# Optimization experiments

Measured on AMD Instinct MI355X. Metric: run time of the kernel, lower is better.

## Reference

```python
import jax, jax.numpy as jnp
import numpy as np

IN_DIM = 768
OUT_DIM = 768


def setup_inputs() -> dict:
    key = jax.random.key(0)
    k_x, k_q, k_k, k_v = jax.random.split(key, 4)
    B, S = 4, 4096
    x = jax.random.normal(k_x, (B, S, IN_DIM), dtype=jnp.float32)
    scale = 1.0 / np.sqrt(IN_DIM)
    Wq = jax.random.normal(k_q, (IN_DIM, OUT_DIM), dtype=jnp.float32) * scale
    Wk = jax.random.normal(k_k, (IN_DIM, OUT_DIM), dtype=jnp.float32) * scale
    Wv = jax.random.normal(k_v, (IN_DIM, OUT_DIM), dtype=jnp.float32) * scale
    return {"x": x, "Wq": Wq, "Wk": Wk, "Wv": Wv}


def reference(x, Wq, Wk, Wv):
    # x: [B, S, D_in]; W*: [D_in, D_out] (Linear without bias)
    q = jnp.einsum('bsd,de->bse', x, Wq)
    k = jnp.einsum('bsd,de->bse', x, Wk)
    v = jnp.einsum('bsd,de->bse', x, Wv)
    S = x.shape[1]
    scores = jnp.einsum('bqe,bke->bqk', q, k)  # [B, S, S]
    causal = jnp.tril(jnp.ones((S, S), dtype=bool))  # True where allowed
    scores = jnp.where(causal[None], scores, -jnp.inf)
    scale = 1.0 / jnp.sqrt(jnp.asarray(q.shape[-1], dtype=scores.dtype))
    weights = jax.nn.softmax(scores * scale, axis=-1)
    # dropout p=0.0 -> identity
    return jnp.einsum('bqk,bke->bqe', weights, v)
```

## Files before the change

kernel.cpp:

```cpp
#include <hip/hip_runtime.h>
#include <hip/hip_bf16.h>
#include <hip/hip_fp16.h>

#define DIM 768
#define SLEN 4096
#define BATCH 4
#define NTILES 528
#define NT256 136

typedef __attribute__((ext_vector_type(8))) short short8;
typedef __attribute__((ext_vector_type(4))) short short4v;
typedef __attribute__((ext_vector_type(4))) float f32x4;
typedef __attribute__((ext_vector_type(8))) _Float16 f16x8;

typedef __attribute__((address_space(1))) void gvoid;
typedef __attribute__((address_space(3))) void lvoid;

__device__ __forceinline__ void gl_lds16(const void* g, void* l) {
  __builtin_amdgcn_global_load_lds((gvoid*)g, (lvoid*)l, 16, 0, 0);
}

__device__ __forceinline__ unsigned short f2h(float x) {
  union { _Float16 h; unsigned short u; } c; c.h = (_Float16)x; return c.u;
}
__device__ __forceinline__ float h2f(unsigned short u) {
  union { _Float16 h; unsigned short u; } c; c.u = u; return (float)c.h;
}

union V8 { short8 v; unsigned short u[8]; };

__global__ __launch_bounds__(256) void convert_x_kernel(
    const float* __restrict__ x, unsigned short* __restrict__ xb) {
  size_t i = ((size_t)blockIdx.x * 256 + threadIdx.x) * 8;
  f32x4 a = *(const f32x4*)(x + i);
  f32x4 b = *(const f32x4*)(x + i + 4);
  V8 o;
#pragma unroll
  for (int j = 0; j < 4; ++j) { o.u[j] = f2h(a[j]); o.u[4 + j] = f2h(b[j]); }
  *(short8*)(xb + i) = o.v;
}

__global__ __launch_bounds__(256) void transpose_w_kernel(
    const float* __restrict__ Wq, const float* __restrict__ Wk,
    const float* __restrict__ Wv, unsigned short* __restrict__ Wt) {
  __shared__ float Tl[32][33];
  const float* Wi = blockIdx.z == 0 ? Wq : (blockIdx.z == 1 ? Wk : Wv);
  unsigned short* Wo = Wt + (size_t)blockIdx.z * DIM * DIM;
  int k0 = blockIdx.x * 32, n0 = blockIdx.y * 32;
  int t = threadIdx.x;
  int r = t >> 3, c4 = (t & 7) * 4;
  f32x4 v = *(const f32x4*)(Wi + (size_t)(k0 + r) * DIM + n0 + c4);
#pragma unroll
  for (int j = 0; j < 4; ++j) Tl[r][c4 + j] = v[j];
  __syncthreads();
  short4v ov;
#pragma unroll
  for (int j = 0; j < 4; ++j) ov[j] = (short)f2h(Tl[c4 + j][r]);
  *(short4v*)(Wo + (size_t)(n0 + r) * DIM + k0 + c4) = ov;
}


#define STAGE(src, row0, kb, ldsoff)                                              \
  {                                                                               \
    gl_lds16((src) + (size_t)((row0) + rA) * DIM + (kb) + cA,                     \
             ldsb + (ldsoff) + t * 16);                                           \
    gl_lds16((src) + (size_t)((row0) + 64 + rA) * DIM + (kb) + cA,                \
             ldsb + (ldsoff) + 8192 + t * 16);                                    \
  }

#define QPHASE(MH, CHB, STG, VMW)                                                 \
  {                                                                               \
    f16x8 afr[4];                                                                 \
    _Pragma("unroll") for (int j = 0; j < 4; ++j)                                 \
        afr[j] = __builtin_bit_cast(f16x8, *(const short8*)(ldsb + aB +           \
                 (MH) * 16384 + (j * 32 + arow) * 128 + (CHB)));                  \
    if ((MH) == 0) {                                                              \
      _Pragma("unroll") for (int n = 0; n < 4; ++n)                               \
          bfr[n] = __builtin_bit_cast(f16x8, *(const short8*)(ldsb + bB +         \
                   bh * 16384 + (brow + n * 16) * 128 + (CHB)));                  \
    }                                                                             \
    STG;                                                                          \
    VMW;                                                                          \
    asm volatile("s_barrier" ::: "memory");                                       \
    asm volatile("s_waitcnt lgkmcnt(0)" ::: "memory");                            \
    __builtin_amdgcn_sched_barrier(0);                                            \
    __builtin_amdgcn_s_setprio(1);                                                \
    _Pragma("unroll") for (int j = 0; j < 4; ++j)                                 \
      _Pragma("unroll") for (int n = 0; n < 4; ++n)                               \
        acc[(MH) * 4 + j][n] = __builtin_amdgcn_mfma_f32_16x16x32_f16(            \
            afr[j], bfr[n], acc[(MH) * 4 + j][n], 0, 0, 0);                       \
    __builtin_amdgcn_s_setprio(0);                                                \
    __builtin_amdgcn_sched_barrier(0);                                            \
    asm volatile("s_barrier" ::: "memory");                                       \
  }

template <int MODE>
__global__ __launch_bounds__(512, 2) void gemm8_kernel(
    const unsigned short* __restrict__ Ag, const unsigned short* __restrict__ Bg,
    unsigned short* __restrict__ o0, unsigned short* __restrict__ o1,
    unsigned short* __restrict__ o2, size_t stAB, size_t stS) {
  __shared__ __align__(16) unsigned short lds[65536];
  char* ldsb = (char*)lds;
  const int t = threadIdx.x;
  const int lane = t & 63, w = t >> 6;
  const int l15 = lane & 15, lg = lane >> 4;
  const int wr = w >> 2, wc = w & 3;

  int m0, n0, qt = 0, kt = 0;
  const unsigned short *A, *B;
  unsigned short* Co = nullptr;
  unsigned short* Sb = nullptr;
  if (MODE == 0) {
    m0 = blockIdx.x * 256; n0 = blockIdx.y * 256;
    A = Ag; B = Bg + (size_t)blockIdx.z * DIM * DIM;
    Co = blockIdx.z == 0 ? o0 : (blockIdx.z == 1 ? o1 : o2);
  } else {
    const int i = blockIdx.x, b = blockIdx.y;
    qt = (int)((sqrtf(8.f * i + 1.f) - 1.f) * 0.5f);
    while ((qt + 1) * (qt + 2) / 2 <= i) ++qt;
    while (qt * (qt + 1) / 2 > i) --qt;
    kt = i - qt * (qt + 1) / 2;
    m0 = qt * 256; n0 = kt * 256;
    A = Ag + (size_t)b * stAB; B = Bg + (size_t)b * stAB;
    Sb = o0 + (size_t)b * stS;
  }

  const int rA = t >> 3;
  const int cA = (((t & 7) ^ ((t >> 3) & 7)) << 3);
  const int ch0 = ((lg ^ (l15 & 7)) << 4);
  const int arow = wr * 16 + l15;
  const int bh = wc >> 1;
  const int brow = (wc & 1) * 64 + l15;

  f32x4 acc[8][4];
#pragma unroll
  for (int f = 0; f < 8; ++f)
#pragma unroll
    for (int n = 0; n < 4; ++n) acc[f][n] = f32x4{0.f, 0.f, 0.f, 0.f};

  STAGE(A, m0, 0, 0);
  STAGE(B, n0, 0, 65536);
  STAGE(B, n0 + 128, 0, 65536 + 16384);
  STAGE(A, m0 + 128, 0, 16384);
  STAGE(A, m0, 64, 32768);
  asm volatile("s_waitcnt vmcnt(4)" ::: "memory");
  asm volatile("s_barrier" ::: "memory");

  for (int tt = 0; tt < 12; ++tt) {
    const int bt = tt & 1;
    const int aB = bt * 32768;
    const int bB = 65536 + bt * 32768;
    const int aN = (1 - bt) * 32768;
    const int bN = 65536 + (1 - bt) * 32768;
    const int kb1 = (tt + 1 < 12 ? tt + 1 : 11) * 64;
    const int kb2 = (tt + 2 < 12 ? tt + 2 : 11) * 64;
    f16x8 bfr[4];
    QPHASE(0, ch0, STAGE(B, n0, kb1, bN),
           asm volatile("s_waitcnt vmcnt(4)" ::: "memory"));
    QPHASE(1, ch0, STAGE(B, n0 + 128, kb1, bN + 16384), (void)0);
    QPHASE(0, ch0 ^ 64, STAGE(A, m0 + 128, kb1, aN + 16384), (void)0);
    QPHASE(1, ch0 ^ 64, STAGE(A, m0, kb2, aB),
           asm volatile("s_waitcnt vmcnt(4)" ::: "memory"));
  }
  asm volatile("s_waitcnt vmcnt(0)" ::: "memory");

  if (MODE == 0) {
#pragma unroll
    for (int f = 0; f < 8; ++f) {
      const int row = m0 + f * 32 + wr * 16 + lg * 4;
#pragma unroll
      for (int n = 0; n < 4; ++n) {
        const int col = n0 + wc * 64 + n * 16 + l15;
#pragma unroll
        for (int ii = 0; ii < 4; ++ii)
          Co[(size_t)(row + ii) * DIM + col] = f2h(acc[f][n][ii]);
      }
    }
  } else {
#pragma unroll
    for (int f = 0; f < 8; ++f) {
      const int rl = (f * 32 + wr * 16 + lg * 4) & 127;
      const int Q128 = qt * 2 + (f >= 4 ? 1 : 0);
      const int K128 = kt * 2 + (wc >> 1);
      if (K128 > Q128) continue;
      const size_t tb = (size_t)(Q128 * (Q128 + 1) / 2 + K128) * 16384;
#pragma unroll
      for (int n = 0; n < 4; ++n) {
        const int cl = ((wc & 1) * 64 + n * 16 + l15);
#pragma unroll
        for (int ii = 0; ii < 4; ++ii)
          Sb[tb + (size_t)(rl + ii) * 128 + cl] = f2h(acc[f][n][ii]);
      }
    }
  }
}

__global__ __launch_bounds__(256) void transpose_v_kernel(
    const unsigned short* __restrict__ Vn, unsigned short* __restrict__ Vt) {
  __shared__ unsigned short T[64][72];
  const int s0 = blockIdx.x * 64, e0 = blockIdx.y * 64;
  const size_t bo = (size_t)blockIdx.z * SLEN * DIM;
  const int t = threadIdx.x;
  const int r = t >> 2, c = (t & 3) * 16;
  V8 v0, v1;
  v0.v = *(const short8*)(Vn + bo + (size_t)(s0 + r) * DIM + e0 + c);
  v1.v = *(const short8*)(Vn + bo + (size_t)(s0 + r) * DIM + e0 + c + 8);
#pragma unroll
  for (int j = 0; j < 8; ++j) { T[r][c + j] = v0.u[j]; T[r][c + 8 + j] = v1.u[j]; }
  __syncthreads();
  unsigned short* Ob = Vt + (size_t)blockIdx.z * DIM * SLEN;
  V8 o0, o1;
#pragma unroll
  for (int j = 0; j < 8; ++j) { o0.u[j] = T[c + j][r]; o1.u[j] = T[c + 8 + j][r]; }
  *(short8*)(Ob + (size_t)(e0 + r) * SLEN + s0 + c) = o0.v;
  *(short8*)(Ob + (size_t)(e0 + r) * SLEN + s0 + c + 8) = o1.v;
}

__global__ __launch_bounds__(256) void gemm_v128_kernel(
    const unsigned short* __restrict__ xb, const unsigned short* __restrict__ wt,
    unsigned short* __restrict__ Vt) {
  __shared__ __align__(16) unsigned short lds[128 * 136];
  unsigned short* As = lds;
  unsigned short* Bs = lds + 4096;
  const int t = threadIdx.x, lane = t & 63, w = t >> 6;
  const int l15 = lane & 15, lg = lane >> 4;
  const int wm = w >> 1, wn = w & 1;
  const int m0 = blockIdx.x * 128, n0 = blockIdx.y * 128;
  const unsigned short* B = wt + (size_t)2 * DIM * DIM;
  f32x4 acc[4][4];
#pragma unroll
  for (int a = 0; a < 4; ++a)
#pragma unroll
    for (int b2 = 0; b2 < 4; ++b2) acc[a][b2] = f32x4{0.f, 0.f, 0.f, 0.f};
  const int c0 = t, c1 = t + 256;
  const int r0 = c0 >> 2, k80 = (c0 & 3) * 8;
  const int r1 = c1 >> 2, k81 = (c1 & 3) * 8;
  for (int kb = 0; kb < DIM; kb += 32) {
    __syncthreads();
    gl_lds16(xb + (size_t)(m0 + r0) * DIM + kb + k80, As + (size_t)c0 * 8);
    gl_lds16(xb + (size_t)(m0 + r1) * DIM + kb + k81, As + (size_t)c1 * 8);
    gl_lds16(B + (size_t)(n0 + r0) * DIM + kb + k80, Bs + (size_t)c0 * 8);
    gl_lds16(B + (size_t)(n0 + r1) * DIM + kb + k81, Bs + (size_t)c1 * 8);
    __syncthreads();
    f16x8 a[4], bf[4];
#pragma unroll
    for (int mi = 0; mi < 4; ++mi)
      a[mi] = __builtin_bit_cast(f16x8, *(const short8*)(As + (wm * 64 + mi * 16 + l15) * 32 + lg * 8));
#pragma unroll
    for (int ni = 0; ni < 4; ++ni)
      bf[ni] = __builtin_bit_cast(f16x8, *(const short8*)(Bs + (wn * 64 + ni * 16 + l15) * 32 + lg * 8));
#pragma unroll
    for (int mi = 0; mi < 4; ++mi)
#pragma unroll
      for (int ni = 0; ni < 4; ++ni)
        acc[mi][ni] = __builtin_amdgcn_mfma_f32_16x16x32_f16(a[mi], bf[ni], acc[mi][ni], 0, 0, 0);
  }
  __syncthreads();
  unsigned short* T = lds;
#pragma unroll
  for (int mi = 0; mi < 4; ++mi)
#pragma unroll
    for (int ni = 0; ni < 4; ++ni)
#pragma unroll
      for (int ii = 0; ii < 4; ++ii) {
        int sl = wm * 64 + mi * 16 + lg * 4 + ii;
        int nl = wn * 64 + ni * 16 + l15;
        T[nl * 136 + sl] = f2h(acc[mi][ni][ii]);
      }
  __syncthreads();
  int bidx = m0 >> 12;
  int s0 = m0 & (SLEN - 1);
  unsigned short* O = Vt + (size_t)bidx * DIM * SLEN;
  int nr = t >> 1, hf = t & 1;
#pragma unroll
  for (int j = 0; j < 8; ++j)
    *(short8*)(O + (size_t)(n0 + nr) * SLEN + s0 + hf * 64 + j * 8) =
        *(const short8*)(T + nr * 136 + hf * 64 + j * 8);
}

__global__ __launch_bounds__(256) void softmax_kernel(
    unsigned short* __restrict__ S, size_t s_bstride) {
  __shared__ float redm[4], reds[4];
  const int r = blockIdx.x, b = blockIdx.y;
  unsigned short* Sb = S + (size_t)b * s_bstride;
  const int qt = r >> 7, rl = r & 127;
  const int ncols = (qt + 1) * 128;
  const size_t rowbase = (size_t)(qt * (qt + 1) / 2) * 16384 + (size_t)rl * 128;
  const int t = threadIdx.x, lane = t & 63, w = t >> 6;
  const int c0 = t * 16;
  const bool act = c0 < ncols;
  const float NEG = -3.0e38f;
  float sv[16];
  unsigned short* p = nullptr;
  if (act) {
    int ktile = c0 >> 7, cl = c0 & 127;
    p = Sb + rowbase + (size_t)ktile * 16384 + cl;
    V8 v0, v1; v0.v = *(const short8*)p; v1.v = *(const short8*)(p + 8);
#pragma unroll
    for (int j = 0; j < 8; ++j) {
      sv[j] = (c0 + j > r) ? NEG : h2f(v0.u[j]);
      sv[8 + j] = (c0 + 8 + j > r) ? NEG : h2f(v1.u[j]);
    }
  } else {
#pragma unroll
    for (int j = 0; j < 16; ++j) sv[j] = NEG;
  }
  float mx = NEG;
#pragma unroll
  for (int j = 0; j < 16; ++j) mx = fmaxf(mx, sv[j]);
#pragma unroll
  for (int d = 1; d < 64; d <<= 1) mx = fmaxf(mx, __shfl_xor(mx, d));
  if (lane == 0) redm[w] = mx;
  __syncthreads();
  mx = fmaxf(fmaxf(redm[0], redm[1]), fmaxf(redm[2], redm[3]));
  const float scl = 1.4426950408889634f / 27.712812921102035f;
  float e[16], sm = 0.f;
#pragma unroll
  for (int j = 0; j < 16; ++j) { e[j] = exp2f((sv[j] - mx) * scl); sm += e[j]; }
#pragma unroll
  for (int d = 1; d < 64; d <<= 1) sm += __shfl_xor(sm, d);
  if (lane == 0) reds[w] = sm;
  __syncthreads();
  float inv = 1.0f / (reds[0] + reds[1] + reds[2] + reds[3]);
  if (act) {
    V8 o0, o1;
#pragma unroll
    for (int j = 0; j < 8; ++j) { o0.u[j] = f2h(e[j] * inv); o1.u[j] = f2h(e[8 + j] * inv); }
    *(short8*)p = o0.v;
    *(short8*)(p + 8) = o1.v;
  }
}

__global__ __launch_bounds__(256) void gemm_pv_kernel(
    const unsigned short* __restrict__ S, const unsigned short* __restrict__ Vt,
    float* __restrict__ Out, size_t s_bstride, int nb) {
  __shared__ __align__(16) unsigned short As[4096], Bs[4096];
  const int idx = blockIdx.x;
  const int qtr = idx / (6 * nb);
  const int rem = idx - qtr * 6 * nb;
  const int b = rem / 6, nt = rem % 6;
  const int qt = 31 - qtr;
  const unsigned short* Sb = S + (size_t)b * s_bstride + (size_t)(qt * (qt + 1) / 2) * 16384;
  const unsigned short* Vb = Vt + (size_t)b * DIM * SLEN + (size_t)(nt * 128) * SLEN;
  float* Ob = Out + (size_t)b * SLEN * DIM + (size_t)(qt * 128) * DIM + nt * 128;
  const int t = threadIdx.x, lane = t & 63, w = t >> 6;
  const int l15 = lane & 15, lg = lane >> 4;
  const int wm = w >> 1, wn = w & 1;
  f32x4 acc[4][4];
#pragma unroll
  for (int a = 0; a < 4; ++a)
#pragma unroll
    for (int b2 = 0; b2 < 4; ++b2) acc[a][b2] = f32x4{0.f, 0.f, 0.f, 0.f};
  const int c0 = t, c1 = t + 256;
  const int r0 = c0 >> 2, k80 = (c0 & 3) * 8;
  const int r1 = c1 >> 2, k81 = (c1 & 3) * 8;
  const int ksteps = (qt + 1) * 4;
  for (int ks = 0; ks < ksteps; ++ks) {
    const int kb = ks * 32;
    const size_t atile = (size_t)(kb >> 7) * 16384 + (size_t)(kb & 127);
    __syncthreads();
    gl_lds16(Sb + atile + (size_t)r0 * 128 + k80, As + (size_t)c0 * 8);
    gl_lds16(Sb + atile + (size_t)r1 * 128 + k81, As + (size_t)c1 * 8);
    gl_lds16(Vb + (size_t)r0 * SLEN + kb + k80, Bs + (size_t)c0 * 8);
    gl_lds16(Vb + (size_t)r1 * SLEN + kb + k81, Bs + (size_t)c1 * 8);
    __syncthreads();
    f16x8 a[4], bf[4];
#pragma unroll
    for (int mi = 0; mi < 4; ++mi)
      a[mi] = __builtin_bit_cast(f16x8, *(const short8*)(As + (wm * 64 + mi * 16 + l15) * 32 + lg * 8));
#pragma unroll
    for (int ni = 0; ni < 4; ++ni)
      bf[ni] = __builtin_bit_cast(f16x8, *(const short8*)(Bs + (wn * 64 + ni * 16 + l15) * 32 + lg * 8));
#pragma unroll
    for (int mi = 0; mi < 4; ++mi)
#pragma unroll
      for (int ni = 0; ni < 4; ++ni)
        acc[mi][ni] = __builtin_amdgcn_mfma_f32_16x16x32_f16(a[mi], bf[ni], acc[mi][ni], 0, 0, 0);
  }
#pragma unroll
  for (int mi = 0; mi < 4; ++mi)
#pragma unroll
    for (int ni = 0; ni < 4; ++ni)
#pragma unroll
      for (int ii = 0; ii < 4; ++ii) {
        int rl = wm * 64 + mi * 16 + lg * 4 + ii;
        int cl = wn * 64 + ni * 16 + l15;
        Ob[(size_t)rl * DIM + cl] = acc[mi][ni][ii];
      }
}

extern "C" void kernel_launch(void* const* d_in, const int* in_sizes, int n_in,
                              void* d_out, int out_size, void* d_ws, size_t ws_size,
                              hipStream_t stream) {
  const float* x  = (const float*)d_in[0];
  const float* Wq = (const float*)d_in[1];
  const float* Wk = (const float*)d_in[2];
  const float* Wv = (const float*)d_in[3];
  float* out = (float*)d_out;

  const size_t n_x = (size_t)BATCH * SLEN * DIM;
  const size_t S_PB = (size_t)NTILES * 16384;
  unsigned short* Q  = (unsigned short*)d_ws;
  unsigned short* K  = Q + n_x;
  unsigned short* Vt = K + n_x;
  unsigned short* xb = Vt + n_x;
  unsigned short* wt = xb + n_x;
  const size_t base_elems = 4 * n_x + (size_t)3 * DIM * DIM;
  const bool full = ws_size >= (base_elems + 4 * S_PB) * 2;

  convert_x_kernel<<<dim3((unsigned)(n_x / 8 / 256)), 256, 0, stream>>>(x, xb);
  transpose_w_kernel<<<dim3(DIM / 32, DIM / 32, 3), 256, 0, stream>>>(Wq, Wk, Wv, wt);

  if (full) {
    unsigned short* S = (unsigned short*)d_ws + base_elems;
    unsigned short* Vn = S;
    gemm8_kernel<0><<<dim3(64, 3, 3), 512, 0, stream>>>(xb, wt, Q, K, Vn, 0, 0);
    transpose_v_kernel<<<dim3(SLEN / 64, DIM / 64, BATCH), 256, 0, stream>>>(Vn, Vt);
    gemm8_kernel<1><<<dim3(NT256, BATCH), 512, 0, stream>>>(
        Q, K, S, nullptr, nullptr, (size_t)SLEN * DIM, S_PB);
    softmax_kernel<<<dim3(SLEN, BATCH), 256, 0, stream>>>(S, S_PB);
    gemm_pv_kernel<<<dim3(32 * 6 * BATCH), 256, 0, stream>>>(S, Vt, out, S_PB, BATCH);
  } else {
    gemm8_kernel<0><<<dim3(64, 3, 2), 512, 0, stream>>>(xb, wt, Q, K, nullptr, 0, 0);
    gemm_v128_kernel<<<dim3((BATCH * SLEN) / 128, DIM / 128), 256, 0, stream>>>(xb, wt, Vt);
    unsigned short* S = xb;
    for (int b = 0; b < BATCH; ++b) {
      const size_t qo = (size_t)b * SLEN * DIM;
      gemm8_kernel<1><<<dim3(NT256, 1), 512, 0, stream>>>(
          Q + qo, K + qo, S, nullptr, nullptr, 0, 0);
      softmax_kernel<<<dim3(SLEN, 1), 256, 0, stream>>>(S, 0);
      gemm_pv_kernel<<<dim3(32 * 6), 256, 0, stream>>>(
          S, Vt + (size_t)b * DIM * SLEN, out + qo, 0, 1);
    }
  }
}
```

Measured before the change: 341.2 us.

## Compute V transposed in-GEMM and add load-balanced 256-tile split-K PV kernel

A new GEMM mode computes Wv^T·x^T directly, so V is written already transposed and the separate V-projection-plus-transpose pass goes away. The 128x128 P·V kernel is replaced by a 256x256, 512-thread, LDS-pipelined kernel. It uses a static schedule in which long causal query rows are split along K into two halves, with partial sums reduced by a small follow-up kernel. Masked upper-triangle tiles are read from a zeroed tile placed in the now-free weight buffer, and the partials live in the x buffer. This aims at more data reuse and better load balance in the PV stage, at the cost of an extra reduce pass and more scratch traffic.

Result: faster. 298.8 us (-12.4%).

```diff
diff --git a/kernel.cpp b/kernel.cpp
--- a/kernel.cpp
+++ b/kernel.cpp
@@ -7,6 +7,7 @@
 #define BATCH 4
 #define NTILES 528
 #define NT256 136
+#define SPB ((size_t)NTILES * 16384)
 
 typedef __attribute__((ext_vector_type(8))) short short8;
 typedef __attribute__((ext_vector_type(4))) short short4v;
@@ -65,6 +66,13 @@
     gl_lds16((src) + (size_t)((row0) + rA) * DIM + (kb) + cA,                     \
              ldsb + (ldsoff) + t * 16);                                           \
     gl_lds16((src) + (size_t)((row0) + 64 + rA) * DIM + (kb) + cA,                \
+             ldsb + (ldsoff) + 8192 + t * 16);                                    \
+  }
+
+#define STAGEP(srcp, stride, ldsoff)                                              \
+  {                                                                               \
+    gl_lds16((srcp) + (size_t)rA * (stride) + cA, ldsb + (ldsoff) + t * 16);      \
+    gl_lds16((srcp) + (size_t)(64 + rA) * (stride) + cA,                          \
              ldsb + (ldsoff) + 8192 + t * 16);                                    \
   }
 
@@ -98,7 +106,7 @@
 __global__ __launch_bounds__(512, 2) void gemm8_kernel(
     const unsigned short* __restrict__ Ag, const unsigned short* __restrict__ Bg,
     unsigned short* __restrict__ o0, unsigned short* __restrict__ o1,
-    unsigned short* __restrict__ o2, size_t stAB, size_t stS) {
+    size_t stAB, size_t stS) {
   __shared__ __align__(16) unsigned short lds[65536];
   char* ldsb = (char*)lds;
   const int t = threadIdx.x;
@@ -113,7 +121,11 @@
   if (MODE == 0) {
     m0 = blockIdx.x * 256; n0 = blockIdx.y * 256;
     A = Ag; B = Bg + (size_t)blockIdx.z * DIM * DIM;
-    Co = blockIdx.z == 0 ? o0 : (blockIdx.z == 1 ? o1 : o2);
+    Co = blockIdx.z == 0 ? o0 : o1;
+  } else if (MODE == 2) {
+    m0 = blockIdx.y * 256; n0 = blockIdx.x * 256;
+    A = Ag; B = Bg;
+    Co = o0;
   } else {
     const int i = blockIdx.x, b = blockIdx.y;
     qt = (int)((sqrtf(8.f * i + 1.f) - 1.f) * 0.5f);
@@ -176,6 +188,20 @@
           Co[(size_t)(row + ii) * DIM + col] = f2h(acc[f][n][ii]);
       }
     }
+  } else if (MODE == 2) {
+    const int bb = n0 >> 12;
+    unsigned short* O = Co + (size_t)bb * DIM * SLEN;
+#pragma unroll
+    for (int f = 0; f < 8; ++f) {
+      const int row = m0 + f * 32 + wr * 16 + lg * 4;
+#pragma unroll
+      for (int n = 0; n < 4; ++n) {
+        const int sl = (n0 + wc * 64 + n * 16 + l15) & (SLEN - 1);
+#pragma unroll
+        for (int ii = 0; ii < 4; ++ii)
+          O[(size_t)(row + ii) * SLEN + sl] = f2h(acc[f][n][ii]);
+      }
+    }
   } else {
 #pragma unroll
     for (int f = 0; f < 8; ++f) {
@@ -193,89 +219,6 @@
       }
     }
   }
-}
-
-__global__ __launch_bounds__(256) void transpose_v_kernel(
-    const unsigned short* __restrict__ Vn, unsigned short* __restrict__ Vt) {
-  __shared__ unsigned short T[64][72];
-  const int s0 = blockIdx.x * 64, e0 = blockIdx.y * 64;
-  const size_t bo = (size_t)blockIdx.z * SLEN * DIM;
-  const int t = threadIdx.x;
-  const int r = t >> 2, c = (t & 3) * 16;
-  V8 v0, v1;
-  v0.v = *(const short8*)(Vn + bo + (size_t)(s0 + r) * DIM + e0 + c);
-  v1.v = *(const short8*)(Vn + bo + (size_t)(s0 + r) * DIM + e0 + c + 8);
-#pragma unroll
-  for (int j = 0; j < 8; ++j) { T[r][c + j] = v0.u[j]; T[r][c + 8 + j] = v1.u[j]; }
-  __syncthreads();
-  unsigned short* Ob = Vt + (size_t)blockIdx.z * DIM * SLEN;
-  V8 o0, o1;
-#pragma unroll
-  for (int j = 0; j < 8; ++j) { o0.u[j] = T[c + j][r]; o1.u[j] = T[c + 8 + j][r]; }
-  *(short8*)(Ob + (size_t)(e0 + r) * SLEN + s0 + c) = o0.v;
-  *(short8*)(Ob + (size_t)(e0 + r) * SLEN + s0 + c + 8) = o1.v;
-}
-
-__global__ __launch_bounds__(256) void gemm_v128_kernel(
-    const unsigned short* __restrict__ xb, const unsigned short* __restrict__ wt,
-    unsigned short* __restrict__ Vt) {
-  __shared__ __align__(16) unsigned short lds[128 * 136];
-  unsigned short* As = lds;
-  unsigned short* Bs = lds + 4096;
-  const int t = threadIdx.x, lane = t & 63, w = t >> 6;
-  const int l15 = lane & 15, lg = lane >> 4;
-  const int wm = w >> 1, wn = w & 1;
-  const int m0 = blockIdx.x * 128, n0 = blockIdx.y * 128;
-  const unsigned short* B = wt + (size_t)2 * DIM * DIM;
-  f32x4 acc[4][4];
-#pragma unroll
-  for (int a = 0; a < 4; ++a)
-#pragma unroll
-    for (int b2 = 0; b2 < 4; ++b2) acc[a][b2] = f32x4{0.f, 0.f, 0.f, 0.f};
-  const int c0 = t, c1 = t + 256;
-  const int r0 = c0 >> 2, k80 = (c0 & 3) * 8;
-  const int r1 = c1 >> 2, k81 = (c1 & 3) * 8;
-  for (int kb = 0; kb < DIM; kb += 32) {
-    __syncthreads();
-    gl_lds16(xb + (size_t)(m0 + r0) * DIM + kb + k80, As + (size_t)c0 * 8);
-    gl_lds16(xb + (size_t)(m0 + r1) * DIM + kb + k81, As + (size_t)c1 * 8);
-    gl_lds16(B + (size_t)(n0 + r0) * DIM + kb + k80, Bs + (size_t)c0 * 8);
-    gl_lds16(B + (size_t)(n0 + r1) * DIM + kb + k81, Bs + (size_t)c1 * 8);
-    __syncthreads();
-    f16x8 a[4], bf[4];
-#pragma unroll
-    for (int mi = 0; mi < 4; ++mi)
-      a[mi] = __builtin_bit_cast(f16x8, *(const short8*)(As + (wm * 64 + mi * 16 + l15) * 32 + lg * 8));
-#pragma unroll
-    for (int ni = 0; ni < 4; ++ni)
-      bf[ni] = __builtin_bit_cast(f16x8, *(const short8*)(Bs + (wn * 64 + ni * 16 + l15) * 32 + lg * 8));
-#pragma unroll
-    for (int mi = 0; mi < 4; ++mi)
-#pragma unroll
-      for (int ni = 0; ni < 4; ++ni)
-        acc[mi][ni] = __builtin_amdgcn_mfma_f32_16x16x32_f16(a[mi], bf[ni], acc[mi][ni], 0, 0, 0);
-  }
-  __syncthreads();
-  unsigned short* T = lds;
-#pragma unroll
-  for (int mi = 0; mi < 4; ++mi)
-#pragma unroll
-    for (int ni = 0; ni < 4; ++ni)
-#pragma unroll
-      for (int ii = 0; ii < 4; ++ii) {
-        int sl = wm * 64 + mi * 16 + lg * 4 + ii;
-        int nl = wn * 64 + ni * 16 + l15;
-        T[nl * 136 + sl] = f2h(acc[mi][ni][ii]);
-      }
-  __syncthreads();
-  int bidx = m0 >> 12;
-  int s0 = m0 & (SLEN - 1);
-  unsigned short* O = Vt + (size_t)bidx * DIM * SLEN;
-  int nr = t >> 1, hf = t & 1;
-#pragma unroll
-  for (int j = 0; j < 8; ++j)
-    *(short8*)(O + (size_t)(n0 + nr) * SLEN + s0 + hf * 64 + j * 8) =
-        *(const short8*)(T + nr * 136 + hf * 64 + j * 8);
 }
 
 __global__ __launch_bounds__(256) void softmax_kernel(
@@ -331,6 +274,125 @@
   }
 }
 
+__global__ __launch_bounds__(256) void zero_tile_kernel(unsigned short* __restrict__ z) {
+  ((short8*)z)[blockIdx.x * 256 + threadIdx.x] = short8{0, 0, 0, 0, 0, 0, 0, 0};
+}
+
+__device__ const int pv_mt[24]  = {15,15,7,14,14,13,13,6,12,12,11,11,5,10,10,9,9,4,8,8,3,2,1,0};
+__device__ const int pv_ks0[24] = {0,32,0,0,30,0,28,0,0,26,0,24,0,0,22,0,20,0,0,18,0,0,0,0};
+__device__ const int pv_kl[24]  = {32,32,32,30,30,28,28,28,26,26,24,24,24,22,22,20,20,20,18,18,16,12,8,4};
+__device__ const int pv_sec[24] = {0,1,0,0,1,0,1,0,0,1,0,1,0,0,1,0,1,0,0,1,0,0,0,0};
+
+__global__ __launch_bounds__(512, 2) void pv256_kernel(
+    const unsigned short* __restrict__ S, const unsigned short* __restrict__ Vt,
+    const unsigned short* __restrict__ Zt, float* __restrict__ Out,
+    float* __restrict__ Part) {
+  __shared__ __align__(16) unsigned short lds[65536];
+  char* ldsb = (char*)lds;
+  const int t = threadIdx.x, lane = t & 63, w = t >> 6;
+  const int l15 = lane & 15, lg = lane >> 4;
+  const int wr = w >> 2, wc = w & 3;
+  const int rank = blockIdx.x / 12, sub = blockIdx.x % 12;
+  const int b = sub / 3, nt = sub % 3;
+  const int mt = pv_mt[rank], ks0 = pv_ks0[rank], kl = pv_kl[rank];
+  const int sec = pv_sec[rank];
+  const int q0 = 2 * mt, q1 = 2 * mt + 1;
+  const int kend = ks0 + kl;
+  const unsigned short* Sbb = S + (size_t)b * SPB;
+  const unsigned short* Vb = Vt + (size_t)b * DIM * SLEN + (size_t)(nt * 256) * SLEN;
+
+  auto asrc = [&](int ks, int qh) -> const unsigned short* {
+    const int K128 = ks >> 1;
+    const unsigned short* base =
+        (K128 <= qh) ? Sbb + (size_t)(qh * (qh + 1) / 2 + K128) * 16384 : Zt;
+    return base + (ks & 1) * 64;
+  };
+
+  const int rA = t >> 3;
+  const int cA = (((t & 7) ^ ((t >> 3) & 7)) << 3);
+  const int ch0 = ((lg ^ (l15 & 7)) << 4);
+  const int arow = wr * 16 + l15;
+  const int bh = wc >> 1;
+  const int brow = (wc & 1) * 64 + l15;
+
+  f32x4 acc[8][4];
+#pragma unroll
+  for (int f = 0; f < 8; ++f)
+#pragma unroll
+    for (int n = 0; n < 4; ++n) acc[f][n] = f32x4{0.f, 0.f, 0.f, 0.f};
+
+  const int ksp = (ks0 + 1 < kend) ? ks0 + 1 : kend - 1;
+  STAGEP(asrc(ks0, q0), 128, 0);
+  STAGEP(Vb + (size_t)ks0 * 64, SLEN, 65536);
+  STAGEP(Vb + (size_t)128 * SLEN + (size_t)ks0 * 64, SLEN, 65536 + 16384);
+  STAGEP(asrc(ks0, q1), 128, 16384);
+  STAGEP(asrc(ksp, q0), 128, 32768);
+  asm volatile("s_waitcnt vmcnt(4)" ::: "memory");
+  asm volatile("s_barrier" ::: "memory");
+
+  for (int it = 0; it < kl; ++it) {
+    const int ts = ks0 + it;
+    const int bt = it & 1;
+    const int aB = bt * 32768;
+    const int bB = 65536 + bt * 32768;
+    const int aN = (1 - bt) * 32768;
+    const int bN = 65536 + (1 - bt) * 32768;
+    const int t1 = (ts + 1 < kend) ? ts + 1 : kend - 1;
+    const int t2 = (ts + 2 < kend) ? ts + 2 : kend - 1;
+    f16x8 bfr[4];
+    QPHASE(0, ch0, STAGEP(Vb + (size_t)t1 * 64, SLEN, bN),
+           asm volatile("s_waitcnt vmcnt(4)" ::: "memory"));
+    QPHASE(1, ch0, STAGEP(Vb + (size_t)128 * SLEN + (size_t)t1 * 64, SLEN, bN + 16384),
+           (void)0);
+    QPHASE(0, ch0 ^ 64, STAGEP(asrc(t1, q1), 128, aN + 16384), (void)0);
+    QPHASE(1, ch0 ^ 64, STAGEP(asrc(t2, q0), 128, aB),
+           asm volatile("s_waitcnt vmcnt(4)" ::: "memory"));
+  }
+  asm volatile("s_waitcnt vmcnt(0)" ::: "memory");
+
+  if (!sec) {
+    float* Ob = Out + (size_t)b * SLEN * DIM + (size_t)(mt * 256) * DIM + nt * 256;
+#pragma unroll
+    for (int f = 0; f < 8; ++f) {
+      const int rl = f * 32 + wr * 16 + lg * 4;
+#pragma unroll
+      for (int n = 0; n < 4; ++n) {
+        const int cl = wc * 64 + n * 16 + l15;
+#pragma unroll
+        for (int ii = 0; ii < 4; ++ii)
+          Ob[(size_t)(rl + ii) * DIM + cl] = acc[f][n][ii];
+      }
+    }
+  } else {
+    float* Pb = Part + (size_t)((b * 3 + nt) * 8 + (mt - 8)) * 65536;
+#pragma unroll
+    for (int f = 0; f < 8; ++f) {
+      const int rl = f * 32 + wr * 16 + lg * 4;
+#pragma unroll
+      for (int n = 0; n < 4; ++n) {
+        const int cl = wc * 64 + n * 16 + l15;
+#pragma unroll
+        for (int ii = 0; ii < 4; ++ii)
+          Pb[(size_t)(rl + ii) * 256 + cl] = acc[f][n][ii];
+      }
+    }
+  }
+}
+
+__global__ __launch_bounds__(256) void pv_reduce_kernel(
+    const float* __restrict__ Part, float* __restrict__ Out) {
+  const int bx = blockIdx.x;
+  const int p = bx >> 6;
+  const int within = ((bx & 63) * 256 + threadIdx.x) * 4;
+  const int mt = 8 + (p & 7);
+  const int bnt = p >> 3, b = bnt / 3, nt = bnt % 3;
+  const int r = within >> 8, c = within & 255;
+  float* o = Out + (size_t)b * SLEN * DIM + (size_t)(mt * 256 + r) * DIM + nt * 256 + c;
+  const f32x4 pv = *(const f32x4*)(Part + (size_t)p * 65536 + within);
+  const f32x4 ov = *(const f32x4*)o;
+  *(f32x4*)o = ov + pv;
+}
+
 __global__ __launch_bounds__(256) void gemm_pv_kernel(
     const unsigned short* __restrict__ S, const unsigned short* __restrict__ Vt,
     float* __restrict__ Out, size_t s_bstride, int nb) {
@@ -399,35 +461,35 @@
   float* out = (float*)d_out;
 
   const size_t n_x = (size_t)BATCH * SLEN * DIM;
-  const size_t S_PB = (size_t)NTILES * 16384;
   unsigned short* Q  = (unsigned short*)d_ws;
   unsigned short* K  = Q + n_x;
   unsigned short* Vt = K + n_x;
   unsigned short* xb = Vt + n_x;
   unsigned short* wt = xb + n_x;
   const size_t base_elems = 4 * n_x + (size_t)3 * DIM * DIM;
-  const bool full = ws_size >= (base_elems + 4 * S_PB) * 2;
+  const bool full = ws_size >= (base_elems + 4 * SPB) * 2;
 
   convert_x_kernel<<<dim3((unsigned)(n_x / 8 / 256)), 256, 0, stream>>>(x, xb);
   transpose_w_kernel<<<dim3(DIM / 32, DIM / 32, 3), 256, 0, stream>>>(Wq, Wk, Wv, wt);
 
+  gemm8_kernel<0><<<dim3(64, 3, 2), 512, 0, stream>>>(xb, wt, Q, K, 0, 0);
+  gemm8_kernel<2><<<dim3(64, 3), 512, 0, stream>>>(
+      wt + (size_t)2 * DIM * DIM, xb, Vt, nullptr, 0, 0);
+
   if (full) {
     unsigned short* S = (unsigned short*)d_ws + base_elems;
-    unsigned short* Vn = S;
-    gemm8_kernel<0><<<dim3(64, 3, 3), 512, 0, stream>>>(xb, wt, Q, K, Vn, 0, 0);
-    transpose_v_kernel<<<dim3(SLEN / 64, DIM / 64, BATCH), 256, 0, stream>>>(Vn, Vt);
+    zero_tile_kernel<<<8, 256, 0, stream>>>(wt);
     gemm8_kernel<1><<<dim3(NT256, BATCH), 512, 0, stream>>>(
-        Q, K, S, nullptr, nullptr, (size_t)SLEN * DIM, S_PB);
-    softmax_kernel<<<dim3(SLEN, BATCH), 256, 0, stream>>>(S, S_PB);
-    gemm_pv_kernel<<<dim3(32 * 6 * BATCH), 256, 0, stream>>>(S, Vt, out, S_PB, BATCH);
+        Q, K, S, nullptr, (size_t)SLEN * DIM, SPB);
+    softmax_kernel<<<dim3(SLEN, BATCH), 256, 0, stream>>>(S, SPB);
+    pv256_kernel<<<dim3(288), 512, 0, stream>>>(S, Vt, wt, out, (float*)xb);
+    pv_reduce_kernel<<<dim3(6144), 256, 0, stream>>>((const float*)xb, out);
   } else {
-    gemm8_kernel<0><<<dim3(64, 3, 2), 512, 0, stream>>>(xb, wt, Q, K, nullptr, 0, 0);
-    gemm_v128_kernel<<<dim3((BATCH * SLEN) / 128, DIM / 128), 256, 0, stream>>>(xb, wt, Vt);
     unsigned short* S = xb;
     for (int b = 0; b < BATCH; ++b) {
       const size_t qo = (size_t)b * SLEN * DIM;
       gemm8_kernel<1><<<dim3(NT256, 1), 512, 0, stream>>>(
-          Q + qo, K + qo, S, nullptr, nullptr, 0, 0);
+          Q + qo, K + qo, S, nullptr, 0, 0);
       softmax_kernel<<<dim3(SLEN, 1), 256, 0, stream>>>(S, 0);
       gemm_pv_kernel<<<dim3(32 * 6), 256, 0, stream>>>(
           S, Vt + (size_t)b * DIM * SLEN, out + qo, 0, 1);
```
